# Kernel optimization log

Measured on AMD Instinct MI355X. Metric: run time of the kernel, lower is better.

## Reference

```python
import jax, jax.numpy as jnp
import numpy as np

N, E, F_IN, H, MH, C, G = 100000, 3200000, 128, 32, 64, 10, 64

def _seg_sum(data, ids, num):
    return jax.ops.segment_sum(data, ids, num_segments=num)

def gcn_conv(x, row, col, ew, W, b, n):
    # PyG GCNConv: linear first, then self-loops + symmetric edge-weight norm + scatter-add
    h = x @ W  # [N, H]
    loop = jnp.arange(n)
    r = jnp.concatenate([row, loop])
    c = jnp.concatenate([col, loop])
    w = jnp.concatenate([ew, jnp.ones((n,), dtype=ew.dtype)])
    deg = _seg_sum(w, c, n)
    dinv = jnp.where(deg > 0, jax.lax.rsqrt(deg), 0.0)
    norm = dinv[r] * w * dinv[c]  # [E+N]
    out = _seg_sum(norm[:, None] * h[r], c, n)  # scatter to targets
    return out + b

def setup_inputs():
    key = jax.random.key(0)
    ks = jax.random.split(key, 16)
    inp = {
        "x": jax.random.normal(ks[0], (N, F_IN), dtype=jnp.float32),
        "edge_index": jax.random.randint(ks[1], (2, E), 0, N, dtype=jnp.int64),
        "edge_weight": jax.random.uniform(ks[2], (E,), dtype=jnp.float32),
        "batch": jnp.sort(jax.random.randint(ks[3], (N,), 0, G, dtype=jnp.int64)),
    }
    def lin(k, i, o):
        s = 1.0 / np.sqrt(i)
        k1, k2 = jax.random.split(k)
        return (jax.random.uniform(k1, (i, o), minval=-s, maxval=s, dtype=jnp.float32),
                jax.random.uniform(k2, (o,), minval=-s, maxval=s, dtype=jnp.float32))
    inp["W1"], inp["b1"] = lin(ks[4], F_IN, H)
    inp["W2"], inp["b2"] = lin(ks[5], H, H)
    inp["W3"], inp["b3"] = lin(ks[6], H, H)
    inp["Wm0"], inp["bm0"] = lin(ks[7], H, MH)
    inp["Wm1"], inp["bm1"] = lin(ks[8], MH, MH)
    inp["Wout"], inp["bout"] = lin(ks[9], MH, C)
    return inp

def reference(x, edge_index, edge_weight, batch, W1, b1, W2, b2, W3, b3, Wm0, bm0, Wm1, bm1, Wout, bout):
    row, col = edge_index[0], edge_index[1]
    h = jax.nn.relu(gcn_conv(x, row, col, edge_weight, W1, b1, N))
    h = jax.nn.relu(gcn_conv(h, row, col, edge_weight, W2, b2, N))
    h = gcn_conv(h, row, col, edge_weight, W3, b3, N)
    # global mean pool over graphs
    sums = _seg_sum(h, batch, G)
    counts = _seg_sum(jnp.ones((N,), dtype=h.dtype), batch, G)
    g = sums / jnp.maximum(counts, 1.0)[:, None]
    # dropout p=0.5 is identity at inference (training=False)
    g = jax.nn.relu(g @ Wm0 + bm0)
    g = jax.nn.relu(g @ Wm1 + bm1)
    return g @ Wout + bout
```

## Files before the change

### kernel.cpp

```cpp
#include <hip/hip_runtime.h>

#define NN 100000
#define NE 3200000
#define FIN 128
#define HID 32
#define MH  64
#define NC  10
#define NG  64
#define NBKT 782
#define NBLK 512
#define EPB  (NE / NBLK)
#define SCANL (NBKT * NBLK)
#define SRCMASK 0x1FFFF
#define BCAP 5120

typedef float floatx2 __attribute__((ext_vector_type(2)));

__global__ __launch_bounds__(1024)
void hist_bkt(const int* __restrict__ ei, int* __restrict__ cnt2) {
    __shared__ int h[NBKT];
    int tid = threadIdx.x, blk = blockIdx.x;
    for (int b = tid; b < NBKT; b += 1024) h[b] = 0;
    __syncthreads();
    int base = blk * EPB;
    for (int i = tid; i < EPB; i += 1024)
        atomicAdd(&h[ei[NE + base + i] >> 7], 1);
    __syncthreads();
    for (int b = tid; b < NBKT; b += 1024) cnt2[b * NBLK + blk] = h[b];
}

__global__ void scan_block(const int* __restrict__ in, int* __restrict__ out,
                           int* __restrict__ bsum, int n) {
    __shared__ int lds[256];
    int tid = threadIdx.x;
    int base = blockIdx.x * 1024 + tid * 4;
    int v0 = 0, v1 = 0, v2 = 0, v3 = 0;
    if (base + 0 < n) v0 = in[base + 0];
    if (base + 1 < n) v1 = in[base + 1];
    if (base + 2 < n) v2 = in[base + 2];
    if (base + 3 < n) v3 = in[base + 3];
    int s = v0 + v1 + v2 + v3;
    lds[tid] = s;
    __syncthreads();
    for (int off = 1; off < 256; off <<= 1) {
        int val = (tid >= off) ? lds[tid - off] : 0;
        __syncthreads();
        lds[tid] += val;
        __syncthreads();
    }
    int excl = lds[tid] - s;
    if (tid == 255) bsum[blockIdx.x] = lds[255];
    if (base + 0 < n) out[base + 0] = excl;
    if (base + 1 < n) out[base + 1] = excl + v0;
    if (base + 2 < n) out[base + 2] = excl + v0 + v1;
    if (base + 3 < n) out[base + 3] = excl + v0 + v1 + v2;
}

__global__ void scan_top(int* __restrict__ bsum, int nb, float* __restrict__ sc) {
    int lane = threadIdx.x;
    for (int i = lane; i < NG * HID + NG; i += 64) sc[i] = 0.0f;
    int carry = 0;
    for (int base = 0; base < nb; base += 64) {
        int i = base + lane;
        int orig = (i < nb) ? bsum[i] : 0;
        int v = orig;
#pragma unroll
        for (int off = 1; off < 64; off <<= 1) {
            int t = __shfl_up(v, off, 64);
            if (lane >= off) v += t;
        }
        if (i < nb) bsum[i] = carry + v - orig;
        carry += __shfl(v, 63, 64);
    }
}

__global__ void scan_add(int* __restrict__ data, const int* __restrict__ bsum, int n) {
    int i = blockIdx.x * 256 + threadIdx.x;
    if (i < n) data[i] += bsum[i >> 10];
}

__global__ __launch_bounds__(1024)
void scatter_bkt(const int* __restrict__ ei, const float* __restrict__ ew,
                 const int* __restrict__ cnt2, const int* __restrict__ scanned,
                 int2* __restrict__ tre) {
    __shared__ int2 pay[EPB];
    __shared__ int scur[NBKT];
    __shared__ int hexc[NBKT];
    __shared__ int gbase[NBKT];
    int tid = threadIdx.x, blk = blockIdx.x;
    int myh = 0;
    if (tid < NBKT) {
        myh = cnt2[tid * NBLK + blk];
        gbase[tid] = scanned[tid * NBLK + blk];
        scur[tid] = myh;
    }
    __syncthreads();
    for (int off = 1; off < NBKT; off <<= 1) {
        int v = (tid < NBKT && tid >= off) ? scur[tid - off] : 0;
        __syncthreads();
        if (tid < NBKT) scur[tid] += v;
        __syncthreads();
    }
    if (tid < NBKT) { int ex = scur[tid] - myh; hexc[tid] = ex; scur[tid] = ex; }
    __syncthreads();
    int base = blk * EPB;
    for (int i = tid; i < EPB; i += 1024) {
        int e = base + i;
        int c = ei[NE + e];
        int r = ei[e];
        unsigned int wb = __float_as_uint(ew[e]);
        int b = c >> 7;
        int j = atomicAdd(&scur[b], 1);
        pay[j] = make_int2(r | ((c & 127) << 17) | ((b & 0xFF) << 24),
                           (int)((wb & ~3u) | ((unsigned)b >> 8)));
    }
    __syncthreads();
    for (int j = tid; j < EPB; j += 1024) {
        int2 q = pay[j];
        int b = (int)((((unsigned)q.y & 3u) << 8) | (((unsigned)q.x >> 24) & 0xFFu));
        int pos = gbase[b] + (j - hexc[b]);
        tre[pos] = make_int2(q.x & 0x00FFFFFF, q.y & ~3);
    }
}

__global__ __launch_bounds__(512)
void sort_k(const int2* __restrict__ tre, const int* __restrict__ scanned,
            unsigned int* __restrict__ srn4, int* __restrict__ rowptr,
            float* __restrict__ dinv) {
    __shared__ int2 ed[BCAP];
    __shared__ int h[128];
    __shared__ float dw[128];
    __shared__ int cur[128];
    int b = blockIdx.x, tid = threadIdx.x;
    int base = scanned[b * NBLK];
    int end = (b == NBKT - 1) ? NE : scanned[(b + 1) * NBLK];
    int n = end - base;
    bool staged = (n <= BCAP);
    if (tid < 128) { h[tid] = 0; dw[tid] = 0.f; }
    __syncthreads();
    for (int i = tid; i < n; i += 512) {
        int2 q = tre[base + i];
        if (staged) ed[i] = q;
        int key = (q.x >> 17) & 127;
        atomicAdd(&h[key], 1);
        atomicAdd(&dw[key], __int_as_float(q.y));
    }
    __syncthreads();
    if (tid < 64) {
        int lane = tid;
        int carry = 0;
#pragma unroll
        for (int c = 0; c < 2; ++c) {
            int idx = c * 64 + lane;
            int hv = h[idx];
            int v = hv;
#pragma unroll
            for (int off = 1; off < 64; off <<= 1) {
                int t = __shfl_up(v, off, 64);
                if (lane >= off) v += t;
            }
            cur[idx] = base + carry + v - hv;
            int node = b * 128 + idx;
            if (node < NN) {
                rowptr[node] = base + carry + v;
                dinv[node] = rsqrtf(1.0f + dw[idx]);
            }
            carry += __shfl(v, 63, 64);
        }
    }
    __syncthreads();
    for (int i = tid; i < n; i += 512) {
        int2 q = staged ? ed[i] : tre[base + i];
        int key = (q.x >> 17) & 127;
        int pos = atomicAdd(&cur[key], 1);
        unsigned int wb = (unsigned)q.y;
        wb += 0x7FFFu + ((wb >> 16) & 1u);
        srn4[pos] = (unsigned)(q.x & SRCMASK) | (((wb >> 16) & 0x7FFFu) << 17);
    }
}

template <int IN_DIM, bool RELU_IN>
__global__ __launch_bounds__(256)
void linear_k(const float* __restrict__ in, const float* __restrict__ W,
              const float* __restrict__ dinv, unsigned int* __restrict__ tmp8) {
    constexpr int J4 = IN_DIM / 4;
    constexpr int XSS = J4 + 1;
    __shared__ float4 xs[64 * XSS];
    __shared__ float4 wp[IN_DIM * 8];
    int tid = threadIdx.x;
    for (int idx = tid; idx < IN_DIM * 8; idx += 256) {
        int j = idx >> 3, kg = idx & 7;
        const float* wr = W + j * 32 + kg * 4;
        wp[idx] = make_float4(wr[0], wr[1], wr[2], wr[3]);
    }
    int rbase = blockIdx.x * 64;
    const float4* in4 = (const float4*)in;
    for (int idx = tid; idx < 64 * J4; idx += 256) {
        int row = idx / J4, j4 = idx % J4;
        int grow = rbase + row;
        float4 v = (grow < NN) ? in4[(size_t)grow * J4 + j4]
                               : make_float4(0.f, 0.f, 0.f, 0.f);
        if (RELU_IN) {
            v.x = fmaxf(v.x, 0.f); v.y = fmaxf(v.y, 0.f);
            v.z = fmaxf(v.z, 0.f); v.w = fmaxf(v.w, 0.f);
        }
        xs[row * XSS + j4] = v;
    }
    __syncthreads();
    int kg = tid & 7;
    int rp = tid >> 3;
    int r0 = rbase + 2 * rp;
    if (r0 >= NN) return;
    const float4* x0 = &xs[(2 * rp) * XSS];
    const float4* x1 = &xs[(2 * rp + 1) * XSS];
    float a00 = 0, a01 = 0, a02 = 0, a03 = 0;
    float a10 = 0, a11 = 0, a12 = 0, a13 = 0;
#pragma unroll
    for (int j4 = 0; j4 < J4; ++j4) {
        float4 v0 = x0[j4], v1 = x1[j4];
        const float4* wj = &wp[j4 * 4 * 8 + kg];
        float4 w0 = wj[0], w1 = wj[8], w2 = wj[16], w3 = wj[24];
#define LSTEP(VX0, VX1, W4) \
        a00 = fmaf(VX0, W4.x, a00); a01 = fmaf(VX0, W4.y, a01); \
        a02 = fmaf(VX0, W4.z, a02); a03 = fmaf(VX0, W4.w, a03); \
        a10 = fmaf(VX1, W4.x, a10); a11 = fmaf(VX1, W4.y, a11); \
        a12 = fmaf(VX1, W4.z, a12); a13 = fmaf(VX1, W4.w, a13);
        LSTEP(v0.x, v1.x, w0)
        LSTEP(v0.y, v1.y, w1)
        LSTEP(v0.z, v1.z, w2)
        LSTEP(v0.w, v1.w, w3)
#undef LSTEP
    }
    float d0 = dinv[r0], d1 = dinv[r0 + 1];
    a00 *= d0; a01 *= d0; a02 *= d0; a03 *= d0;
    a10 *= d1; a11 *= d1; a12 *= d1; a13 *= d1;
    int q0 = __builtin_amdgcn_cvt_pk_fp8_f32(a00, a01, 0, false);
    q0 = __builtin_amdgcn_cvt_pk_fp8_f32(a02, a03, q0, true);
    int q1 = __builtin_amdgcn_cvt_pk_fp8_f32(a10, a11, 0, false);
    q1 = __builtin_amdgcn_cvt_pk_fp8_f32(a12, a13, q1, true);
    tmp8[r0 * 8 + kg] = (unsigned int)q0;
    tmp8[(r0 + 1) * 8 + kg] = (unsigned int)q1;
}

#define AGG_BODY \
    int lane = threadIdx.x & 63; \
    int g = lane >> 3; \
    int q = lane & 7; \
    int end = rowptr[wid]; \
    int start = (wid == 0) ? 0 : rowptr[wid - 1]; \
    float a0 = 0, a1 = 0, a2 = 0, a3 = 0; \
    float b0 = 0, b1 = 0, b2 = 0, b3 = 0; \
    int e = start + g; \
    for (; e + 24 < end; e += 32) { \
        unsigned int p0 = srn4[e]; \
        unsigned int p1 = srn4[e + 8]; \
        unsigned int p2 = srn4[e + 16]; \
        unsigned int p3 = srn4[e + 24]; \
        unsigned int u0 = tmp8[(size_t)(p0 & SRCMASK) * 8 + q]; \
        unsigned int u1 = tmp8[(size_t)(p1 & SRCMASK) * 8 + q]; \
        unsigned int u2 = tmp8[(size_t)(p2 & SRCMASK) * 8 + q]; \
        unsigned int u3 = tmp8[(size_t)(p3 & SRCMASK) * 8 + q]; \
        float w0 = __uint_as_float((p0 >> 1) & 0x7FFF0000u); \
        float w1 = __uint_as_float((p1 >> 1) & 0x7FFF0000u); \
        float w2 = __uint_as_float((p2 >> 1) & 0x7FFF0000u); \
        float w3 = __uint_as_float((p3 >> 1) & 0x7FFF0000u); \
        floatx2 lo, hi; \
        lo = __builtin_amdgcn_cvt_pk_f32_fp8(u0, false); \
        hi = __builtin_amdgcn_cvt_pk_f32_fp8(u0, true); \
        a0 = fmaf(w0, lo.x, a0); a1 = fmaf(w0, lo.y, a1); \
        a2 = fmaf(w0, hi.x, a2); a3 = fmaf(w0, hi.y, a3); \
        lo = __builtin_amdgcn_cvt_pk_f32_fp8(u1, false); \
        hi = __builtin_amdgcn_cvt_pk_f32_fp8(u1, true); \
        b0 = fmaf(w1, lo.x, b0); b1 = fmaf(w1, lo.y, b1); \
        b2 = fmaf(w1, hi.x, b2); b3 = fmaf(w1, hi.y, b3); \
        lo = __builtin_amdgcn_cvt_pk_f32_fp8(u2, false); \
        hi = __builtin_amdgcn_cvt_pk_f32_fp8(u2, true); \
        a0 = fmaf(w2, lo.x, a0); a1 = fmaf(w2, lo.y, a1); \
        a2 = fmaf(w2, hi.x, a2); a3 = fmaf(w2, hi.y, a3); \
        lo = __builtin_amdgcn_cvt_pk_f32_fp8(u3, false); \
        hi = __builtin_amdgcn_cvt_pk_f32_fp8(u3, true); \
        b0 = fmaf(w3, lo.x, b0); b1 = fmaf(w3, lo.y, b1); \
        b2 = fmaf(w3, hi.x, b2); b3 = fmaf(w3, hi.y, b3); \
    } \
    for (; e < end; e += 8) { \
        unsigned int p = srn4[e]; \
        unsigned int u = tmp8[(size_t)(p & SRCMASK) * 8 + q]; \
        float w = __uint_as_float((p >> 1) & 0x7FFF0000u); \
        floatx2 lo = __builtin_amdgcn_cvt_pk_f32_fp8(u, false); \
        floatx2 hi = __builtin_amdgcn_cvt_pk_f32_fp8(u, true); \
        a0 = fmaf(w, lo.x, a0); a1 = fmaf(w, lo.y, a1); \
        a2 = fmaf(w, hi.x, a2); a3 = fmaf(w, hi.y, a3); \
    } \
    a0 += b0; a1 += b1; a2 += b2; a3 += b3; \
    a0 += __shfl_xor(a0, 8, 64); a1 += __shfl_xor(a1, 8, 64); \
    a2 += __shfl_xor(a2, 8, 64); a3 += __shfl_xor(a3, 8, 64); \
    a0 += __shfl_xor(a0, 16, 64); a1 += __shfl_xor(a1, 16, 64); \
    a2 += __shfl_xor(a2, 16, 64); a3 += __shfl_xor(a3, 16, 64); \
    a0 += __shfl_xor(a0, 32, 64); a1 += __shfl_xor(a1, 32, 64); \
    a2 += __shfl_xor(a2, 32, 64); a3 += __shfl_xor(a3, 32, 64);

__global__ void aggregate(const unsigned int* __restrict__ srn4,
                          const int* __restrict__ rowptr,
                          const float* __restrict__ dinv,
                          const float* __restrict__ bias,
                          const unsigned int* __restrict__ tmp8,
                          float* __restrict__ h) {
    int wid = (blockIdx.x * 256 + threadIdx.x) >> 6;
    if (wid >= NN) return;
    AGG_BODY
    if (g == 0) {
        float d = dinv[wid];
        unsigned int sv = tmp8[(size_t)wid * 8 + q];
        floatx2 slo = __builtin_amdgcn_cvt_pk_f32_fp8(sv, false);
        floatx2 shi = __builtin_amdgcn_cvt_pk_f32_fp8(sv, true);
        float4 bq = ((const float4*)bias)[q];
        float4 o;
        o.x = bq.x + d * (slo.x + a0);
        o.y = bq.y + d * (slo.y + a1);
        o.z = bq.z + d * (shi.x + a2);
        o.w = bq.w + d * (shi.y + a3);
        ((float4*)(h + (size_t)wid * HID))[q] = o;
    }
}

__global__ void agg_lin(const unsigned int* __restrict__ srn4,
                        const int* __restrict__ rowptr,
                        const float* __restrict__ dinv,
                        const float* __restrict__ bias,
                        const float* __restrict__ Wn,
                        const unsigned int* __restrict__ tmp8,
                        unsigned int* __restrict__ tmp8_out) {
    __shared__ float hrow[4][HID];
    int wid = (blockIdx.x * 256 + threadIdx.x) >> 6;
    if (wid >= NN) return;
    int wv = threadIdx.x >> 6;
    AGG_BODY
    float d = dinv[wid];
    if (g == 0) {
        unsigned int sv = tmp8[(size_t)wid * 8 + q];
        floatx2 slo = __builtin_amdgcn_cvt_pk_f32_fp8(sv, false);
        floatx2 shi = __builtin_amdgcn_cvt_pk_f32_fp8(sv, true);
        float4 bq = ((const float4*)bias)[q];
        float4 o;
        o.x = fmaxf(bq.x + d * (slo.x + a0), 0.f);
        o.y = fmaxf(bq.y + d * (slo.y + a1), 0.f);
        o.z = fmaxf(bq.z + d * (shi.x + a2), 0.f);
        o.w = fmaxf(bq.w + d * (shi.y + a3), 0.f);
        *((float4*)&hrow[wv][4 * q]) = o;
    }
    int j = lane & 31, half = lane >> 5;
    const float* hr = hrow[wv];
    const float* wc = Wn + j;
    float y = 0.f;
#pragma unroll
    for (int k = 0; k < 16; ++k) {
        int kk = half * 16 + k;
        y = fmaf(hr[kk], wc[kk * 32], y);
    }
    y += __shfl_xor(y, 32, 64);
    y *= d;
    float y1 = __shfl_down(y, 1, 64);
    float y2 = __shfl_down(y, 2, 64);
    float y3 = __shfl_down(y, 3, 64);
    if (half == 0 && (j & 3) == 0) {
        int w0 = __builtin_amdgcn_cvt_pk_fp8_f32(y, y1, 0, false);
        w0 = __builtin_amdgcn_cvt_pk_fp8_f32(y2, y3, w0, true);
        tmp8_out[wid * 8 + (j >> 2)] = (unsigned int)w0;
    }
}

__global__ void pool_k(const float* __restrict__ h, const int* __restrict__ batch,
                       float* __restrict__ sums, float* __restrict__ counts) {
    int t = blockIdx.x * 256 + threadIdx.x;
    int chunk = t >> 5, k = t & 31;
    int n0 = chunk * 32;
    if (n0 >= NN) return;
    int n1 = min(n0 + 32, NN);
    int g = batch[n0];
    float acc = 0.f, cacc = 0.f;
    for (int i = n0; i < n1; ++i) {
        int gi = batch[i];
        if (gi != g) {
            atomicAdd(&sums[g * HID + k], acc);
            if (k == 0) atomicAdd(&counts[g], cacc);
            g = gi; acc = 0.f; cacc = 0.f;
        }
        acc += h[(size_t)i * HID + k];
        cacc += 1.f;
    }
    atomicAdd(&sums[g * HID + k], acc);
    if (k == 0) atomicAdd(&counts[g], cacc);
}

__global__ __launch_bounds__(64)
void mlp_k(const float* __restrict__ sums, const float* __restrict__ counts,
           const float* __restrict__ Wm0, const float* __restrict__ bm0,
           const float* __restrict__ Wm1, const float* __restrict__ bm1,
           const float* __restrict__ Wout, const float* __restrict__ bout,
           float* __restrict__ out) {
    __shared__ float g0[HID];
    __shared__ float g1[MH];
    __shared__ float g2[MH];
    int g = blockIdx.x;
    int k = threadIdx.x;
    if (k < HID) g0[k] = sums[g * HID + k] / fmaxf(counts[g], 1.0f);
    __syncthreads();
    float acc = bm0[k];
#pragma unroll
    for (int j = 0; j < HID; ++j) acc = fmaf(g0[j], Wm0[j * MH + k], acc);
    g1[k] = fmaxf(acc, 0.f);
    __syncthreads();
    float acc2 = bm1[k];
#pragma unroll
    for (int j = 0; j < MH; ++j) acc2 = fmaf(g1[j], Wm1[j * MH + k], acc2);
    g2[k] = fmaxf(acc2, 0.f);
    __syncthreads();
    if (k < NC) {
        float acc3 = bout[k];
#pragma unroll
        for (int j = 0; j < MH; ++j) acc3 = fmaf(g2[j], Wout[j * NC + k], acc3);
        out[g * NC + k] = acc3;
    }
}

extern "C" void kernel_launch(void* const* d_in, const int* in_sizes, int n_in,
                              void* d_out, int out_size, void* d_ws, size_t ws_size,
                              hipStream_t stream) {
    const float* x    = (const float*)d_in[0];
    const int*   ei   = (const int*)d_in[1];
    const float* ew   = (const float*)d_in[2];
    const int*   batch= (const int*)d_in[3];
    const float* W1   = (const float*)d_in[4];
    const float* b1   = (const float*)d_in[5];
    const float* W2   = (const float*)d_in[6];
    const float* b2   = (const float*)d_in[7];
    const float* W3   = (const float*)d_in[8];
    const float* b3   = (const float*)d_in[9];
    const float* Wm0  = (const float*)d_in[10];
    const float* bm0  = (const float*)d_in[11];
    const float* Wm1  = (const float*)d_in[12];
    const float* bm1  = (const float*)d_in[13];
    const float* Wout = (const float*)d_in[14];
    const float* bout = (const float*)d_in[15];
    float* out = (float*)d_out;

    char* p = (char*)d_ws;
    unsigned int* srn4 = (unsigned int*)p; p += sizeof(unsigned int) * (size_t)NE;
    char*  S   = p;                      p += 12 * (size_t)NE;
    int2*  tre = (int2*)S;
    int*   cnt2    = (int*)(S + sizeof(int2) * (size_t)NE);
    int*   scanned = cnt2 + SCANL;
    unsigned int* tmp8  = (unsigned int*)S;
    unsigned int* tmp8b = tmp8 + (size_t)NN * 8;
    float* hA  = (float*)(S + 2 * (size_t)NN * HID);
    int*   bsum    = (int*)p;            p += sizeof(int) * 512;
    float* dinv    = (float*)p;          p += sizeof(float) * NN;
    int*   rowptr  = (int*)p;            p += sizeof(int) * NN;
    float* sums    = (float*)p;          p += sizeof(float) * NG * HID;
    float* counts  = (float*)p;

    dim3 blk(256);
    const int NB_SCAN = (SCANL + 1023) / 1024;
    const int NB_LIN = (NN + 63) / 64;

    hist_bkt<<<NBLK, 1024, 0, stream>>>(ei, cnt2);
    scan_block<<<NB_SCAN, blk, 0, stream>>>(cnt2, scanned, bsum, SCANL);
    scan_top<<<1, 64, 0, stream>>>(bsum, NB_SCAN, sums);
    scan_add<<<(SCANL + 255) / 256, blk, 0, stream>>>(scanned, bsum, SCANL);
    scatter_bkt<<<NBLK, 1024, 0, stream>>>(ei, ew, cnt2, scanned, tre);
    sort_k<<<NBKT, 512, 0, stream>>>(tre, scanned, srn4, rowptr, dinv);

    linear_k<FIN, false><<<NB_LIN, blk, 0, stream>>>(x, W1, dinv, tmp8);
    agg_lin<<<25000, blk, 0, stream>>>(srn4, rowptr, dinv, b1, W2, tmp8, tmp8b);
    agg_lin<<<25000, blk, 0, stream>>>(srn4, rowptr, dinv, b2, W3, tmp8b, tmp8);
    aggregate<<<25000, blk, 0, stream>>>(srn4, rowptr, dinv, b3, tmp8, hA);

    pool_k<<<391, blk, 0, stream>>>(hA, batch, sums, counts);
    mlp_k<<<NG, 64, 0, stream>>>(sums, counts, Wm0, bm0, Wm1, bm1, Wout, bout, out);
}
```

Measured before the change: 404.2 us.

## Widen aggregation to 8-byte gathers per lane, replace LDS staging with shuffles

The aggregation wavefront is remapped so each lane loads 8 fp8 features (uint2) instead of 4. That gives 4 lanes per source row and 16 edges in flight per iteration instead of 8 lanes and 8 edges, with 8 accumulators per lane and an extra shuffle-reduction stage. In agg_lin, the shared-memory staging of the hidden row before the 32x32 linear layer is replaced by cross-lane shuffles, which removes the LDS writes and reads. The goal is fewer, wider gather instructions and no LDS traffic. The cost is higher register pressure and more shuffle operations in the reduction.

```diff
diff --git a/kernel.cpp b/kernel.cpp
--- a/kernel.cpp
+++ b/kernel.cpp
@@ -244,60 +244,49 @@
 
 #define AGG_BODY \
     int lane = threadIdx.x & 63; \
-    int g = lane >> 3; \
-    int q = lane & 7; \
+    int sl = lane >> 2; \
+    int oc = lane & 3; \
     int end = rowptr[wid]; \
     int start = (wid == 0) ? 0 : rowptr[wid - 1]; \
-    float a0 = 0, a1 = 0, a2 = 0, a3 = 0; \
-    float b0 = 0, b1 = 0, b2 = 0, b3 = 0; \
-    int e = start + g; \
-    for (; e + 24 < end; e += 32) { \
+    float a0 = 0, a1 = 0, a2 = 0, a3 = 0, a4 = 0, a5 = 0, a6 = 0, a7 = 0; \
+    float c0 = 0, c1 = 0, c2 = 0, c3 = 0, c4 = 0, c5 = 0, c6 = 0, c7 = 0; \
+    int e = start + sl; \
+    for (; e + 16 < end; e += 32) { \
         unsigned int p0 = srn4[e]; \
-        unsigned int p1 = srn4[e + 8]; \
-        unsigned int p2 = srn4[e + 16]; \
-        unsigned int p3 = srn4[e + 24]; \
-        unsigned int u0 = tmp8[(size_t)(p0 & SRCMASK) * 8 + q]; \
-        unsigned int u1 = tmp8[(size_t)(p1 & SRCMASK) * 8 + q]; \
-        unsigned int u2 = tmp8[(size_t)(p2 & SRCMASK) * 8 + q]; \
-        unsigned int u3 = tmp8[(size_t)(p3 & SRCMASK) * 8 + q]; \
+        unsigned int p1 = srn4[e + 16]; \
+        uint2 u0 = *(const uint2*)(tmp8 + (size_t)(p0 & SRCMASK) * 8 + 2 * oc); \
+        uint2 u1 = *(const uint2*)(tmp8 + (size_t)(p1 & SRCMASK) * 8 + 2 * oc); \
         float w0 = __uint_as_float((p0 >> 1) & 0x7FFF0000u); \
         float w1 = __uint_as_float((p1 >> 1) & 0x7FFF0000u); \
-        float w2 = __uint_as_float((p2 >> 1) & 0x7FFF0000u); \
-        float w3 = __uint_as_float((p3 >> 1) & 0x7FFF0000u); \
-        floatx2 lo, hi; \
-        lo = __builtin_amdgcn_cvt_pk_f32_fp8(u0, false); \
-        hi = __builtin_amdgcn_cvt_pk_f32_fp8(u0, true); \
-        a0 = fmaf(w0, lo.x, a0); a1 = fmaf(w0, lo.y, a1); \
-        a2 = fmaf(w0, hi.x, a2); a3 = fmaf(w0, hi.y, a3); \
-        lo = __builtin_amdgcn_cvt_pk_f32_fp8(u1, false); \
-        hi = __builtin_amdgcn_cvt_pk_f32_fp8(u1, true); \
-        b0 = fmaf(w1, lo.x, b0); b1 = fmaf(w1, lo.y, b1); \
-        b2 = fmaf(w1, hi.x, b2); b3 = fmaf(w1, hi.y, b3); \
-        lo = __builtin_amdgcn_cvt_pk_f32_fp8(u2, false); \
-        hi = __builtin_amdgcn_cvt_pk_f32_fp8(u2, true); \
-        a0 = fmaf(w2, lo.x, a0); a1 = fmaf(w2, lo.y, a1); \
-        a2 = fmaf(w2, hi.x, a2); a3 = fmaf(w2, hi.y, a3); \
-        lo = __builtin_amdgcn_cvt_pk_f32_fp8(u3, false); \
-        hi = __builtin_amdgcn_cvt_pk_f32_fp8(u3, true); \
-        b0 = fmaf(w3, lo.x, b0); b1 = fmaf(w3, lo.y, b1); \
-        b2 = fmaf(w3, hi.x, b2); b3 = fmaf(w3, hi.y, b3); \
+        floatx2 f; \
+        f = __builtin_amdgcn_cvt_pk_f32_fp8(u0.x, false); a0 = fmaf(w0, f.x, a0); a1 = fmaf(w0, f.y, a1); \
+        f = __builtin_amdgcn_cvt_pk_f32_fp8(u0.x, true);  a2 = fmaf(w0, f.x, a2); a3 = fmaf(w0, f.y, a3); \
+        f = __builtin_amdgcn_cvt_pk_f32_fp8(u0.y, false); a4 = fmaf(w0, f.x, a4); a5 = fmaf(w0, f.y, a5); \
+        f = __builtin_amdgcn_cvt_pk_f32_fp8(u0.y, true);  a6 = fmaf(w0, f.x, a6); a7 = fmaf(w0, f.y, a7); \
+        f = __builtin_amdgcn_cvt_pk_f32_fp8(u1.x, false); c0 = fmaf(w1, f.x, c0); c1 = fmaf(w1, f.y, c1); \
+        f = __builtin_amdgcn_cvt_pk_f32_fp8(u1.x, true);  c2 = fmaf(w1, f.x, c2); c3 = fmaf(w1, f.y, c3); \
+        f = __builtin_amdgcn_cvt_pk_f32_fp8(u1.y, false); c4 = fmaf(w1, f.x, c4); c5 = fmaf(w1, f.y, c5); \
+        f = __builtin_amdgcn_cvt_pk_f32_fp8(u1.y, true);  c6 = fmaf(w1, f.x, c6); c7 = fmaf(w1, f.y, c7); \
     } \
-    for (; e < end; e += 8) { \
+    for (; e < end; e += 16) { \
         unsigned int p = srn4[e]; \
-        unsigned int u = tmp8[(size_t)(p & SRCMASK) * 8 + q]; \
+        uint2 u = *(const uint2*)(tmp8 + (size_t)(p & SRCMASK) * 8 + 2 * oc); \
         float w = __uint_as_float((p >> 1) & 0x7FFF0000u); \
-        floatx2 lo = __builtin_amdgcn_cvt_pk_f32_fp8(u, false); \
-        floatx2 hi = __builtin_amdgcn_cvt_pk_f32_fp8(u, true); \
-        a0 = fmaf(w, lo.x, a0); a1 = fmaf(w, lo.y, a1); \
-        a2 = fmaf(w, hi.x, a2); a3 = fmaf(w, hi.y, a3); \
+        floatx2 f; \
+        f = __builtin_amdgcn_cvt_pk_f32_fp8(u.x, false); a0 = fmaf(w, f.x, a0); a1 = fmaf(w, f.y, a1); \
+        f = __builtin_amdgcn_cvt_pk_f32_fp8(u.x, true);  a2 = fmaf(w, f.x, a2); a3 = fmaf(w, f.y, a3); \
+        f = __builtin_amdgcn_cvt_pk_f32_fp8(u.y, false); a4 = fmaf(w, f.x, a4); a5 = fmaf(w, f.y, a5); \
+        f = __builtin_amdgcn_cvt_pk_f32_fp8(u.y, true);  a6 = fmaf(w, f.x, a6); a7 = fmaf(w, f.y, a7); \
     } \
-    a0 += b0; a1 += b1; a2 += b2; a3 += b3; \
-    a0 += __shfl_xor(a0, 8, 64); a1 += __shfl_xor(a1, 8, 64); \
-    a2 += __shfl_xor(a2, 8, 64); a3 += __shfl_xor(a3, 8, 64); \
-    a0 += __shfl_xor(a0, 16, 64); a1 += __shfl_xor(a1, 16, 64); \
-    a2 += __shfl_xor(a2, 16, 64); a3 += __shfl_xor(a3, 16, 64); \
-    a0 += __shfl_xor(a0, 32, 64); a1 += __shfl_xor(a1, 32, 64); \
-    a2 += __shfl_xor(a2, 32, 64); a3 += __shfl_xor(a3, 32, 64);
+    a0 += c0; a1 += c1; a2 += c2; a3 += c3; \
+    a4 += c4; a5 += c5; a6 += c6; a7 += c7; \
+    _Pragma("unroll") \
+    for (int m = 4; m <= 32; m <<= 1) { \
+        a0 += __shfl_xor(a0, m, 64); a1 += __shfl_xor(a1, m, 64); \
+        a2 += __shfl_xor(a2, m, 64); a3 += __shfl_xor(a3, m, 64); \
+        a4 += __shfl_xor(a4, m, 64); a5 += __shfl_xor(a5, m, 64); \
+        a6 += __shfl_xor(a6, m, 64); a7 += __shfl_xor(a7, m, 64); \
+    }
 
 __global__ void aggregate(const unsigned int* __restrict__ srn4,
                           const int* __restrict__ rowptr,
@@ -308,18 +297,24 @@
     int wid = (blockIdx.x * 256 + threadIdx.x) >> 6;
     if (wid >= NN) return;
     AGG_BODY
-    if (g == 0) {
+    if (sl == 0) {
         float d = dinv[wid];
-        unsigned int sv = tmp8[(size_t)wid * 8 + q];
-        floatx2 slo = __builtin_amdgcn_cvt_pk_f32_fp8(sv, false);
-        floatx2 shi = __builtin_amdgcn_cvt_pk_f32_fp8(sv, true);
-        float4 bq = ((const float4*)bias)[q];
-        float4 o;
-        o.x = bq.x + d * (slo.x + a0);
-        o.y = bq.y + d * (slo.y + a1);
-        o.z = bq.z + d * (shi.x + a2);
-        o.w = bq.w + d * (shi.y + a3);
-        ((float4*)(h + (size_t)wid * HID))[q] = o;
+        uint2 sv = *(const uint2*)(tmp8 + (size_t)wid * 8 + 2 * oc);
+        float4 bq0 = ((const float4*)bias)[2 * oc];
+        float4 bq1 = ((const float4*)bias)[2 * oc + 1];
+        floatx2 f;
+        float4 o0, o1;
+        f = __builtin_amdgcn_cvt_pk_f32_fp8(sv.x, false);
+        o0.x = bq0.x + d * (f.x + a0); o0.y = bq0.y + d * (f.y + a1);
+        f = __builtin_amdgcn_cvt_pk_f32_fp8(sv.x, true);
+        o0.z = bq0.z + d * (f.x + a2); o0.w = bq0.w + d * (f.y + a3);
+        f = __builtin_amdgcn_cvt_pk_f32_fp8(sv.y, false);
+        o1.x = bq1.x + d * (f.x + a4); o1.y = bq1.y + d * (f.y + a5);
+        f = __builtin_amdgcn_cvt_pk_f32_fp8(sv.y, true);
+        o1.z = bq1.z + d * (f.x + a6); o1.w = bq1.w + d * (f.y + a7);
+        float4* hp = (float4*)(h + (size_t)wid * HID);
+        hp[2 * oc] = o0;
+        hp[2 * oc + 1] = o1;
     }
 }
 
@@ -330,33 +325,44 @@
                         const float* __restrict__ Wn,
                         const unsigned int* __restrict__ tmp8,
                         unsigned int* __restrict__ tmp8_out) {
-    __shared__ float hrow[4][HID];
     int wid = (blockIdx.x * 256 + threadIdx.x) >> 6;
     if (wid >= NN) return;
-    int wv = threadIdx.x >> 6;
     AGG_BODY
     float d = dinv[wid];
-    if (g == 0) {
-        unsigned int sv = tmp8[(size_t)wid * 8 + q];
-        floatx2 slo = __builtin_amdgcn_cvt_pk_f32_fp8(sv, false);
-        floatx2 shi = __builtin_amdgcn_cvt_pk_f32_fp8(sv, true);
-        float4 bq = ((const float4*)bias)[q];
-        float4 o;
-        o.x = fmaxf(bq.x + d * (slo.x + a0), 0.f);
-        o.y = fmaxf(bq.y + d * (slo.y + a1), 0.f);
-        o.z = fmaxf(bq.z + d * (shi.x + a2), 0.f);
-        o.w = fmaxf(bq.w + d * (shi.y + a3), 0.f);
-        *((float4*)&hrow[wv][4 * q]) = o;
-    }
+    uint2 sv = *(const uint2*)(tmp8 + (size_t)wid * 8 + 2 * oc);
+    float4 bq0 = ((const float4*)bias)[2 * oc];
+    float4 bq1 = ((const float4*)bias)[2 * oc + 1];
+    floatx2 f;
+    float h0, h1, h2, h3, h4, h5, h6, h7;
+    f = __builtin_amdgcn_cvt_pk_f32_fp8(sv.x, false);
+    h0 = fmaxf(bq0.x + d * (f.x + a0), 0.f); h1 = fmaxf(bq0.y + d * (f.y + a1), 0.f);
+    f = __builtin_amdgcn_cvt_pk_f32_fp8(sv.x, true);
+    h2 = fmaxf(bq0.z + d * (f.x + a2), 0.f); h3 = fmaxf(bq0.w + d * (f.y + a3), 0.f);
+    f = __builtin_amdgcn_cvt_pk_f32_fp8(sv.y, false);
+    h4 = fmaxf(bq1.x + d * (f.x + a4), 0.f); h5 = fmaxf(bq1.y + d * (f.y + a5), 0.f);
+    f = __builtin_amdgcn_cvt_pk_f32_fp8(sv.y, true);
+    h6 = fmaxf(bq1.z + d * (f.x + a6), 0.f); h7 = fmaxf(bq1.w + d * (f.y + a7), 0.f);
     int j = lane & 31, half = lane >> 5;
-    const float* hr = hrow[wv];
-    const float* wc = Wn + j;
+    int srcA = (lane & 60) | (half << 1);
+    int srcB = srcA | 1;
+    const float* wc = Wn + (half << 9) + j;
     float y = 0.f;
-#pragma unroll
-    for (int k = 0; k < 16; ++k) {
-        int kk = half * 16 + k;
-        y = fmaf(hr[kk], wc[kk * 32], y);
-    }
+    y = fmaf(__shfl(h0, srcA, 64), wc[0 * 32], y);
+    y = fmaf(__shfl(h1, srcA, 64), wc[1 * 32], y);
+    y = fmaf(__shfl(h2, srcA, 64), wc[2 * 32], y);
+    y = fmaf(__shfl(h3, srcA, 64), wc[3 * 32], y);
+    y = fmaf(__shfl(h4, srcA, 64), wc[4 * 32], y);
+    y = fmaf(__shfl(h5, srcA, 64), wc[5 * 32], y);
+    y = fmaf(__shfl(h6, srcA, 64), wc[6 * 32], y);
+    y = fmaf(__shfl(h7, srcA, 64), wc[7 * 32], y);
+    y = fmaf(__shfl(h0, srcB, 64), wc[8 * 32], y);
+    y = fmaf(__shfl(h1, srcB, 64), wc[9 * 32], y);
+    y = fmaf(__shfl(h2, srcB, 64), wc[10 * 32], y);
+    y = fmaf(__shfl(h3, srcB, 64), wc[11 * 32], y);
+    y = fmaf(__shfl(h4, srcB, 64), wc[12 * 32], y);
+    y = fmaf(__shfl(h5, srcB, 64), wc[13 * 32], y);
+    y = fmaf(__shfl(h6, srcB, 64), wc[14 * 32], y);
+    y = fmaf(__shfl(h7, srcB, 64), wc[15 * 32], y);
     y += __shfl_xor(y, 32, 64);
     y *= d;
     float y1 = __shfl_down(y, 1, 64);
```

Measured after the change: 417.1 us. 1.03x slower.
